# Kernel optimization log

Hardware: AMD Instinct MI355X
Metric: run time of the kernel (lower is better)

## Reference

```python
import jax, jax.numpy as jnp
import numpy as np

M, K, N = 8192, 4096, 4096


def setup_inputs() -> dict:
    key = jax.random.key(0)
    k1, k2, k3, k4, k5 = jax.random.split(key, 5)
    x = jax.random.randint(k1, (M, K), -127, 128, dtype=jnp.int32).astype(jnp.int8)
    weight_int8 = jax.random.randint(k2, (N, K), -127, 128, dtype=jnp.int32).astype(jnp.int8)
    scale_x = jax.random.uniform(k3, (M,), dtype=jnp.float32, minval=0.001, maxval=0.02)
    scale_w = jnp.abs(jax.random.normal(k4, (N,), dtype=jnp.float32)) * 0.01
    bias = (jax.random.normal(k5, (N,), dtype=jnp.float32) * 0.01).astype(jnp.float16)
    return {"x": x, "scale_x": scale_x, "weight_int8": weight_int8,
            "scale_w": scale_w, "bias": bias}


def reference(x, scale_x, weight_int8, scale_w, bias):
    # int8 GEMM with int32 accumulation: acc[M,N] = x @ weight^T
    acc = jnp.matmul(x, weight_int8.T, preferred_element_type=jnp.int32)
    inv_127_sq = jnp.float32(1.0 / (127.0 * 127.0))
    scale_w_eff = scale_w * inv_127_sq                      # [N]
    out = acc.astype(jnp.float32) * scale_x[:, None] * scale_w_eff[None, :]
    out = out + bias.astype(jnp.float32)[None, :]
    return out.astype(jnp.float16)
```

## Files before the change

### kernel.cpp

```cpp
#include <hip/hip_runtime.h>
#include <stdint.h>

#define M_DIM 8192
#define K_DIM 4096
#define N_DIM 4096

typedef __attribute__((ext_vector_type(4))) int v4i;

__device__ __forceinline__ int pack4(v4i v) {
    return (int)(((uint32_t)v.x & 0xffu)
               | (((uint32_t)v.y & 0xffu) << 8)
               | (((uint32_t)v.z & 0xffu) << 16)
               | (((uint32_t)v.w & 0xffu) << 24));
}

__global__ __launch_bounds__(256) void pack_ab(
    const int* __restrict__ srcA, const int* __restrict__ srcB,
    int* __restrict__ dstA, int* __restrict__ dstB,
    int aGroups)
{
    int g = blockIdx.x * 256 + threadIdx.x;
    const v4i* src;
    int* dst;
    if (g < aGroups) { src = (const v4i*)srcA; dst = dstA; }
    else             { src = (const v4i*)srcB; dst = dstB; g -= aGroups; }
    dst[g] = pack4(src[g]);
}

__device__ __forceinline__ void gload16(const void* g, void* lds) {
    __builtin_amdgcn_global_load_lds(
        (__attribute__((address_space(1))) void*)(g),
        (__attribute__((address_space(3))) void*)(lds),
        16, 0, 0);
}

__global__ __launch_bounds__(256) void int8_gemm_dequant(
    const int8_t* __restrict__ A,
    const float*  __restrict__ scale_x,
    const int8_t* __restrict__ W,
    const float*  __restrict__ scale_w,
    const float*  __restrict__ bias,
    float*        __restrict__ out)
{
    __shared__ __align__(16) int8_t Alds[128 * 64];
    __shared__ __align__(16) int8_t Blds[128 * 64];

    const int t    = threadIdx.x;
    const int lane = t & 63;
    const int w    = t >> 6;
    const int wm   = w >> 1;
    const int wn   = w & 1;

    const int m0 = blockIdx.y * 128;
    const int n0 = blockIdx.x * 128;

    const int row_s = t >> 2;
    const int cgb   = (t & 3) * 16;

    const int8_t* Ag = A + (size_t)(m0 + row_s) * K_DIM + cgb;
    const int8_t* Bg = W + (size_t)(n0 + row_s) * K_DIM + cgb;
    int8_t* Ad = &Alds[t * 16];
    int8_t* Bd = &Blds[t * 16];

    const v4i* Alds4 = (const v4i*)Alds;
    const v4i* Blds4 = (const v4i*)Blds;
    const int rA  = wm * 64 + (lane & 15);
    const int rB  = wn * 64 + (lane & 15);
    const int cg0 = lane >> 4;

    v4i acc[4][4] = {};

    for (int k0 = 0; k0 < K_DIM; k0 += 64) {
        gload16(Ag + k0,                       Ad);
        gload16(Ag + k0 + (size_t)64 * K_DIM, Ad + 4096);
        gload16(Bg + k0,                       Bd);
        gload16(Bg + k0 + (size_t)64 * K_DIM, Bd + 4096);
        __syncthreads();

        v4i a[4], b[4];
#pragma unroll
        for (int i = 0; i < 4; ++i) a[i] = Alds4[(rA + i * 16) * 4 + cg0];
#pragma unroll
        for (int j = 0; j < 4; ++j) b[j] = Blds4[(rB + j * 16) * 4 + cg0];

#pragma unroll
        for (int i = 0; i < 4; ++i)
#pragma unroll
            for (int j = 0; j < 4; ++j)
                acc[i][j] = __builtin_amdgcn_mfma_i32_16x16x64_i8(
                    a[i], b[j], acc[i][j], 0, 0, 0);

        __syncthreads();
    }

    const int col = lane & 15;
    const int rq  = (lane >> 4) * 4;
    const float inv127sq = 1.0f / (127.0f * 127.0f);

    float sx[4][4];
#pragma unroll
    for (int i = 0; i < 4; ++i)
#pragma unroll
        for (int r = 0; r < 4; ++r)
            sx[i][r] = scale_x[m0 + wm * 64 + i * 16 + rq + r];

#pragma unroll
    for (int j = 0; j < 4; ++j) {
        const int n  = n0 + wn * 64 + j * 16 + col;
        const float sw = scale_w[n] * inv127sq;
        const float bf = bias[n];
#pragma unroll
        for (int i = 0; i < 4; ++i) {
            const int mrow = m0 + wm * 64 + i * 16 + rq;
#pragma unroll
            for (int r = 0; r < 4; ++r) {
                out[(size_t)(mrow + r) * N_DIM + n] =
                    (float)acc[i][j][r] * sx[i][r] * sw + bf;
            }
        }
    }
}

extern "C" void kernel_launch(void* const* d_in, const int* in_sizes, int n_in,
                              void* d_out, int out_size, void* d_ws, size_t ws_size,
                              hipStream_t stream) {
    const int*   x_i32   = (const int*)  d_in[0];
    const float* scale_x = (const float*)d_in[1];
    const int*   w_i32   = (const int*)  d_in[2];
    const float* scale_w = (const float*)d_in[3];
    const float* bias    = (const float*)d_in[4];
    float* out = (float*)d_out;

    int8_t* A8 = (int8_t*)d_ws;
    int8_t* B8 = A8 + (size_t)M_DIM * K_DIM;

    const int a_groups = (M_DIM * K_DIM) / 4;
    const int b_groups = (N_DIM * K_DIM) / 4;
    const int total    = a_groups + b_groups;
    pack_ab<<<total / 256, 256, 0, stream>>>(x_i32, w_i32, (int*)A8, (int*)B8,
                                             a_groups);

    dim3 grid(N_DIM / 128, M_DIM / 128);
    int8_gemm_dequant<<<grid, 256, 0, stream>>>(A8, scale_x, B8, scale_w, bias, out);
}
```

Baseline: 432.1 us.

## Rewrite int8 GEMM as 256x256 tiled, double-buffered 8-wave pipelined kernel

Replaces the 128x128 single-buffered GEMM with a 256x256 tile computed by 8 waves. The K dimension runs through a double-buffered 128 KB LDS pipeline that issues async global-to-LDS loads alongside the MFMA phases. It also adds XOR swizzling of LDS columns against bank conflicts, s_setprio around the MFMA blocks, and a workgroup index remap for L2 locality. This targets the per-iteration barrier stalls and memory latency of the old kernel, in exchange for heavy LDS use (one block per CU) and more register pressure from the 32 accumulators.

```diff
diff --git a/kernel.cpp b/kernel.cpp
--- a/kernel.cpp
+++ b/kernel.cpp
@@ -27,14 +27,14 @@
     dst[g] = pack4(src[g]);
 }
 
-__device__ __forceinline__ void gload16(const void* g, void* lds) {
+__device__ __forceinline__ void gload16(const void* g, void* lds_p) {
     __builtin_amdgcn_global_load_lds(
         (__attribute__((address_space(1))) void*)(g),
-        (__attribute__((address_space(3))) void*)(lds),
+        (__attribute__((address_space(3))) void*)(lds_p),
         16, 0, 0);
 }
 
-__global__ __launch_bounds__(256) void int8_gemm_dequant(
+__global__ __launch_bounds__(512, 2) void int8_gemm_dequant(
     const int8_t* __restrict__ A,
     const float*  __restrict__ scale_x,
     const int8_t* __restrict__ W,
@@ -42,83 +42,151 @@
     const float*  __restrict__ bias,
     float*        __restrict__ out)
 {
-    __shared__ __align__(16) int8_t Alds[128 * 64];
-    __shared__ __align__(16) int8_t Blds[128 * 64];
+    __shared__ __align__(16) int8_t lds[131072];
 
     const int t    = threadIdx.x;
     const int lane = t & 63;
     const int w    = t >> 6;
-    const int wm   = w >> 1;
-    const int wn   = w & 1;
-
-    const int m0 = blockIdx.y * 128;
-    const int n0 = blockIdx.x * 128;
-
-    const int row_s = t >> 2;
-    const int cgb   = (t & 3) * 16;
-
-    const int8_t* Ag = A + (size_t)(m0 + row_s) * K_DIM + cgb;
-    const int8_t* Bg = W + (size_t)(n0 + row_s) * K_DIM + cgb;
-    int8_t* Ad = &Alds[t * 16];
-    int8_t* Bd = &Blds[t * 16];
-
-    const v4i* Alds4 = (const v4i*)Alds;
-    const v4i* Blds4 = (const v4i*)Blds;
-    const int rA  = wm * 64 + (lane & 15);
-    const int rB  = wn * 64 + (lane & 15);
-    const int cg0 = lane >> 4;
-
-    v4i acc[4][4] = {};
-
-    for (int k0 = 0; k0 < K_DIM; k0 += 64) {
-        gload16(Ag + k0,                       Ad);
-        gload16(Ag + k0 + (size_t)64 * K_DIM, Ad + 4096);
-        gload16(Bg + k0,                       Bd);
-        gload16(Bg + k0 + (size_t)64 * K_DIM, Bd + 4096);
-        __syncthreads();
-
-        v4i a[4], b[4];
-#pragma unroll
-        for (int i = 0; i < 4; ++i) a[i] = Alds4[(rA + i * 16) * 4 + cg0];
-#pragma unroll
-        for (int j = 0; j < 4; ++j) b[j] = Blds4[(rB + j * 16) * 4 + cg0];
-
-#pragma unroll
-        for (int i = 0; i < 4; ++i)
-#pragma unroll
-            for (int j = 0; j < 4; ++j)
-                acc[i][j] = __builtin_amdgcn_mfma_i32_16x16x64_i8(
-                    a[i], b[j], acc[i][j], 0, 0, 0);
-
-        __syncthreads();
+    const int wm   = w >> 2;
+    const int wn   = w & 3;
+
+    const int wg  = blockIdx.x;
+    const int swz = (wg & 7) * 64 + (wg >> 3);
+    const int n0  = (swz & 15) * 256;
+    const int m0  = (swz >> 4) * 256;
+
+    const int srow = t >> 2;
+    const int scg  = (t & 3) ^ ((t >> 3) & 3);
+    const int8_t* Ap = A + (size_t)(m0 + srow) * K_DIM + scg * 16;
+    const int8_t* Bp = W + (size_t)(n0 + srow) * K_DIM + scg * 16;
+    int8_t* ldsb = &lds[t * 16];
+
+    const int rd = (lane & 15) * 64 + (((lane >> 4) ^ ((lane >> 1) & 3)) * 16);
+
+    v4i acc[8][4] = {};
+    v4i afr[4], bfr[4];
+
+#define HOFF(buf, mat, ksh) ((((buf) << 2) | ((mat) << 1) | (ksh)) << 14)
+
+#define STAGE(buf, mat, ksh, OFF) do {                                        \
+    const int8_t* _g = ((mat) ? Bp : Ap) + (OFF) + (ksh) * 64;                \
+    int8_t* _d = ldsb + HOFF(buf, mat, ksh);                                  \
+    gload16(_g, _d);                                                          \
+    gload16(_g + (size_t)128 * K_DIM, _d + 8192);                             \
+} while (0)
+
+#define READ_B(buf, ksh) do {                                                 \
+    const int8_t* _p = lds + HOFF(buf, 1, ksh) + wn * 4096 + rd;              \
+    bfr[0] = *(const v4i*)(_p);                                               \
+    bfr[1] = *(const v4i*)(_p + 1024);                                        \
+    bfr[2] = *(const v4i*)(_p + 2048);                                        \
+    bfr[3] = *(const v4i*)(_p + 3072);                                        \
+} while (0)
+
+#define READ_A(buf, ksh, qm) do {                                             \
+    const int8_t* _p = lds + HOFF(buf, 0, ksh) + wm * 8192 + (qm) * 4096 + rd;\
+    afr[0] = *(const v4i*)(_p);                                               \
+    afr[1] = *(const v4i*)(_p + 1024);                                        \
+    afr[2] = *(const v4i*)(_p + 2048);                                        \
+    afr[3] = *(const v4i*)(_p + 3072);                                        \
+} while (0)
+
+#define MFMA_Q(qm) do {                                                       \
+    _Pragma("unroll")                                                         \
+    for (int mt = 0; mt < 4; ++mt) {                                          \
+        _Pragma("unroll")                                                     \
+        for (int nt = 0; nt < 4; ++nt) {                                      \
+            acc[(qm) * 4 + mt][nt] = __builtin_amdgcn_mfma_i32_16x16x64_i8(   \
+                afr[mt], bfr[nt], acc[(qm) * 4 + mt][nt], 0, 0, 0);           \
+        }                                                                     \
+    }                                                                         \
+} while (0)
+
+#define NOWAIT ((void)0)
+#define WAIT4  asm volatile("s_waitcnt vmcnt(4)" ::: "memory")
+#define WAIT0  asm volatile("s_waitcnt vmcnt(0)" ::: "memory")
+#define NOSTG  ((void)0)
+
+#define PHASE(DO_RB, buf, ksh, qm, STG, WAITV) do {                           \
+    if (DO_RB) { READ_B(buf, ksh); }                                          \
+    READ_A(buf, ksh, qm);                                                     \
+    STG;                                                                      \
+    __builtin_amdgcn_s_barrier();                                             \
+    asm volatile("s_waitcnt lgkmcnt(0)" ::: "memory");                        \
+    __builtin_amdgcn_s_setprio(1);                                            \
+    MFMA_Q(qm);                                                               \
+    __builtin_amdgcn_s_setprio(0);                                            \
+    WAITV;                                                                    \
+    __builtin_amdgcn_s_barrier();                                             \
+} while (0)
+
+    STAGE(0, 1, 0, 0);   STAGE(0, 0, 0, 0);
+    STAGE(0, 1, 1, 0);   STAGE(0, 0, 1, 0);
+    STAGE(1, 1, 0, 128); STAGE(1, 0, 0, 128);
+    WAIT4;
+    __builtin_amdgcn_s_barrier();
+
+    for (int i = 0; i < 15; ++i) {
+        PHASE(1, 0, 0, 0, STAGE(1, 1, 1, 128), NOWAIT);
+        PHASE(0, 0, 0, 1, STAGE(1, 0, 1, 128), NOWAIT);
+        PHASE(1, 0, 1, 0, STAGE(0, 1, 0, 256), NOWAIT);
+        PHASE(0, 0, 1, 1, STAGE(0, 0, 0, 256), WAIT4);
+        PHASE(1, 1, 0, 0, STAGE(0, 1, 1, 256), NOWAIT);
+        PHASE(0, 1, 0, 1, STAGE(0, 0, 1, 256), NOWAIT);
+        PHASE(1, 1, 1, 0, STAGE(1, 1, 0, 384), NOWAIT);
+        PHASE(0, 1, 1, 1, STAGE(1, 0, 0, 384), WAIT4);
+        Ap += 256; Bp += 256;
     }
+
+    PHASE(1, 0, 0, 0, STAGE(1, 1, 1, 128), NOWAIT);
+    PHASE(0, 0, 0, 1, STAGE(1, 0, 1, 128), NOWAIT);
+    PHASE(1, 0, 1, 0, NOSTG, NOWAIT);
+    PHASE(0, 0, 1, 1, NOSTG, WAIT0);
+    PHASE(1, 1, 0, 0, NOSTG, NOWAIT);
+    PHASE(0, 1, 0, 1, NOSTG, NOWAIT);
+    PHASE(1, 1, 1, 0, NOSTG, NOWAIT);
+    PHASE(0, 1, 1, 1, NOSTG, NOWAIT);
 
     const int col = lane & 15;
     const int rq  = (lane >> 4) * 4;
     const float inv127sq = 1.0f / (127.0f * 127.0f);
-
-    float sx[4][4];
-#pragma unroll
-    for (int i = 0; i < 4; ++i)
-#pragma unroll
-        for (int r = 0; r < 4; ++r)
-            sx[i][r] = scale_x[m0 + wm * 64 + i * 16 + rq + r];
+    const int mbase = m0 + wm * 128;
+    const int nbase = n0 + wn * 64;
+
+    float sx[8][4];
+#pragma unroll
+    for (int ii = 0; ii < 8; ++ii) {
+        const int mrow = mbase + (ii >> 2) * 64 + (ii & 3) * 16 + rq;
+#pragma unroll
+        for (int r = 0; r < 4; ++r) sx[ii][r] = scale_x[mrow + r];
+    }
 
 #pragma unroll
     for (int j = 0; j < 4; ++j) {
-        const int n  = n0 + wn * 64 + j * 16 + col;
+        const int n  = nbase + j * 16 + col;
         const float sw = scale_w[n] * inv127sq;
         const float bf = bias[n];
 #pragma unroll
-        for (int i = 0; i < 4; ++i) {
-            const int mrow = m0 + wm * 64 + i * 16 + rq;
+        for (int ii = 0; ii < 8; ++ii) {
+            const int mrow = mbase + (ii >> 2) * 64 + (ii & 3) * 16 + rq;
 #pragma unroll
             for (int r = 0; r < 4; ++r) {
                 out[(size_t)(mrow + r) * N_DIM + n] =
-                    (float)acc[i][j][r] * sx[i][r] * sw + bf;
+                    (float)acc[ii][j][r] * sx[ii][r] * sw + bf;
             }
         }
     }
+
+#undef HOFF
+#undef STAGE
+#undef READ_B
+#undef READ_A
+#undef MFMA_Q
+#undef NOWAIT
+#undef WAIT4
+#undef WAIT0
+#undef NOSTG
+#undef PHASE
 }
 
 extern "C" void kernel_launch(void* const* d_in, const int* in_sizes, int n_in,
@@ -140,6 +208,5 @@
     pack_ab<<<total / 256, 256, 0, stream>>>(x_i32, w_i32, (int*)A8, (int*)B8,
                                              a_groups);
 
-    dim3 grid(N_DIM / 128, M_DIM / 128);
-    int8_gemm_dequant<<<grid, 256, 0, stream>>>(A8, scale_x, B8, scale_w, bias, out);
-}
+    int8_gemm_dequant<<<512, 512, 0, stream>>>(A8, scale_x, B8, scale_w, bias, out);
+}
```

New measurement: 401.0 us. 1.08x faster.
